# Kernel tuning notes

Hardware: AMD Instinct MI355X
Metric: run time of the kernel (lower is better)

The kernel has to match this reference:

```python
import math
import jax
import jax.numpy as jnp
import numpy as np

N_ATOMS = 5000
N_EDGES = 100000
FEAT = 128
BERN_K = 16
R_CUT = 5.0
EPS = 1e-15


def _swish(x, a, b):
    # learnable swish: alpha * x * sigmoid(beta * x)
    return a * x * jax.nn.sigmoid(b * x)


def _y_all(r_ij, r, l):
    """Real spherical harmonics of the unit vector r_ij/r, all m in [-l, l]."""
    x, y, z = r_ij[:, 0], r_ij[:, 1], r_ij[:, 2]
    if l == 0:
        return jnp.ones((r_ij.shape[0], 1), r_ij.dtype)
    if l == 1:
        return jnp.stack([y, z, x], axis=1) / r
    s3 = math.sqrt(3.0)
    r2 = (r * r)[:, 0]
    return jnp.stack(
        [s3 * x * y, s3 * y * z, 1.5 * z * z - 0.5 * r2, s3 * x * z, 0.5 * s3 * (x * x - y * y)],
        axis=1,
    ) / r2[:, None]


def _rho_k(r, gamma, K):
    """Bernstein radial basis b_{k,K-1}(exp(-gamma r)) times SpookyNet smooth cutoff."""
    rr = r[:, 0]
    g = jnp.maximum(gamma, 0.0)  # gamma.clamp(0)
    e = jnp.exp(-g * rr)[:, None]  # [E,1]
    k = jnp.arange(K)
    binom = jnp.asarray([math.comb(K - 1, i) for i in range(K)], dtype=r.dtype)
    bern = binom * e ** k * (1.0 - e) ** (K - 1 - k)  # [E,K]
    safe = jnp.where(rr < R_CUT, (R_CUT - rr) * (R_CUT + rr), 1.0)
    fcut = jnp.where(rr < R_CUT, jnp.exp(-rr * rr / safe), 0.0)
    return bern * fcut[:, None]


def _forward(xyz, x_tilde, rm_W1, rm_b1, rm_W2, rm_b2, rm_W3, rm_b3,
             rl_W1, rl_b1, rl_W2, rl_b2, rl_W3, rl_b3,
             G_s, G_p, G_d, P_1, P_2, D_1, D_2,
             gamma_s, gamma_p, gamma_d, sw_alpha, sw_beta, nbrs):
    n = xyz.shape[0]
    sw = lambda t, i: _swish(t, sw_alpha[i], sw_beta[i])
    # batched pre-activation linear over channel dim c
    bl = lambda W, b, t: jnp.einsum('cij,cnj->cni', W, t) + b[:, None, :]

    # BatchedResidualMLP on x_tilde repeated over 4 channels
    x4 = jnp.broadcast_to(x_tilde, (4,) + x_tilde.shape)  # [4,N,F]
    h = x4 + bl(rm_W2, rm_b2, sw(bl(rm_W1, rm_b1, sw(x4, 0)), 1))
    res_outs = x4 + bl(rm_W3, rm_b3, sw(h, 2))  # [4,N,F]

    i0, i1 = nbrs[:, 0], nbrs[:, 1]
    r_ij = xyz[i1] - xyz[i0]  # [E,3]
    r = jnp.sqrt((r_ij ** 2 + EPS).sum(-1, keepdims=True))  # stable norm, [E,1]
    K = G_s.shape[1]

    def quant(l, gamma, G, res_out):
        # g: [E,K,2l+1] = rho_k outer y_lm
        g = _rho_k(r, gamma, K)[:, :, None] * _y_all(r_ij, r, l)[:, None, :]
        mm = jnp.einsum('fk,ekm->efm', G, g)  # [E,F,2l+1]
        per = res_out[i1][:, :, None] * mm
        return jax.ops.segment_sum(per, i0, num_segments=n)  # scatter_add -> [N,F,2l+1]

    q_s = quant(0, gamma_s, G_s, res_outs[1])
    q_p = quant(1, gamma_p, G_p, res_outs[2])
    q_d = quant(2, gamma_d, G_d, res_outs[3])

    def inner(q, M1, M2):
        t1 = jnp.einsum('ij,njm->nim', M1, q)
        t2 = jnp.einsum('ij,njm->nim', M2, q)
        return (t1 * t2).sum(-1)

    inp = res_outs[0] + q_s[:, :, 0] + inner(q_p, P_1, P_2) + inner(q_d, D_1, D_2)

    # ResidualMLP (note: no outer skip, matching the torch code)
    lin = lambda W, b, t: t @ W.T + b
    h2 = inp + lin(rl_W2, rl_b2, sw(lin(rl_W1, rl_b1, sw(inp, 3)), 4))
    return lin(rl_W3, rl_b3, sw(h2, 5))


def setup_inputs():
    key = jax.random.key(0)
    ks = jax.random.split(key, 24)
    p = lambda k, shape: jax.random.normal(k, shape, dtype=jnp.float32) * 0.1
    F, K = FEAT, BERN_K
    return {
        'xyz': jax.random.normal(ks[0], (N_ATOMS, 3), jnp.float32) * 3.0,
        'x_tilde': jax.random.normal(ks[1], (N_ATOMS, F), jnp.float32),
        'nbrs': jax.random.randint(ks[2], (N_EDGES, 2), 0, N_ATOMS),
        'rm_W1': p(ks[3], (4, F, F)), 'rm_b1': p(ks[4], (4, F)),
        'rm_W2': p(ks[5], (4, F, F)), 'rm_b2': p(ks[6], (4, F)),
        'rm_W3': p(ks[7], (4, F, F)), 'rm_b3': p(ks[8], (4, F)),
        'rl_W1': p(ks[9], (F, F)), 'rl_b1': p(ks[10], (F,)),
        'rl_W2': p(ks[11], (F, F)), 'rl_b2': p(ks[12], (F,)),
        'rl_W3': p(ks[13], (F, F)), 'rl_b3': p(ks[14], (F,)),
        'G_s': p(ks[15], (F, K)), 'G_p': p(ks[16], (F, K)), 'G_d': p(ks[17], (F, K)),
        'P_1': p(ks[18], (F, F)), 'P_2': p(ks[19], (F, F)),
        'D_1': p(ks[20], (F, F)), 'D_2': p(ks[21], (F, F)),
        'gamma_s': jnp.asarray(0.5, jnp.float32),
        'gamma_p': jnp.asarray(0.5, jnp.float32),
        'gamma_d': jnp.asarray(0.5, jnp.float32),
        'sw_alpha': jnp.ones((6,), jnp.float32),
        'sw_beta': jnp.full((6,), 1.702, jnp.float32),
    }


def reference(xyz, x_tilde, nbrs, rm_W1, rm_b1, rm_W2, rm_b2, rm_W3, rm_b3,
              rl_W1, rl_b1, rl_W2, rl_b2, rl_W3, rl_b3,
              G_s, G_p, G_d, P_1, P_2, D_1, D_2,
              gamma_s, gamma_p, gamma_d, sw_alpha, sw_beta):
    return _forward(xyz, x_tilde, rm_W1, rm_b1, rm_W2, rm_b2, rm_W3, rm_b3,
                    rl_W1, rl_b1, rl_W2, rl_b2, rl_W3, rl_b3,
                    G_s, G_p, G_d, P_1, P_2, D_1, D_2,
                    gamma_s, gamma_p, gamma_d, sw_alpha, sw_beta, nbrs)
```

## Files before the change

### kernel.cpp

```cpp
#include <hip/hip_runtime.h>
#include <hip/hip_bf16.h>
#include <math.h>

#define NA 5000
#define NE 100000
#define F 128
#define KB 16
#define RCUT 5.0f
#define RECW 28
#define QCAP 40

typedef long long i64;
typedef __attribute__((ext_vector_type(8))) short bf16x8;
typedef __attribute__((ext_vector_type(4))) float f32x4;

__device__ __forceinline__ float swish_f(float t, float a, float b){
    return a * t / (1.0f + __expf(-b * t));
}
__device__ __forceinline__ float bf2f(unsigned short u){
    return __uint_as_float(((unsigned)u) << 16);
}
__device__ __forceinline__ unsigned short f2bf(float x){
    unsigned b = __float_as_uint(x);
    return (unsigned short)((b + 0x8000u) >> 16);
}
__device__ __forceinline__ unsigned pack2(float a, float b){
    return (unsigned)f2bf(a) | ((unsigned)f2bf(b) << 16);
}
__device__ __forceinline__ int swz(int row, int byte_in_row){
    return row * 256 + (byte_in_row ^ ((row & 7) << 4));
}

template<int MT>
__device__ __forceinline__ void gemm_stage(const unsigned short* __restrict__ Wb,
                                           const short* act_lds, f32x4 (&acc)[MT][2],
                                           int lane, int wave)
{
    bf16x8 B[2][4], A[MT][4];
    const int cl = lane & 15, kh = lane >> 4;
    #pragma unroll
    for (int ntl = 0; ntl < 2; ++ntl){
        const unsigned short* wp = Wb + (i64)(wave * 32 + ntl * 16 + cl) * F + kh * 8;
        #pragma unroll
        for (int kb = 0; kb < 4; ++kb)
            B[ntl][kb] = *(const bf16x8*)(wp + kb * 32);
    }
    #pragma unroll
    for (int mt = 0; mt < MT; ++mt){
        int row = mt * 16 + cl;
        #pragma unroll
        for (int kb = 0; kb < 4; ++kb)
            A[mt][kb] = *(const bf16x8*)((const char*)act_lds + swz(row, kb * 64 + kh * 16));
    }
    #pragma unroll
    for (int mt = 0; mt < MT; ++mt)
        #pragma unroll
        for (int ntl = 0; ntl < 2; ++ntl)
            #pragma unroll
            for (int kb = 0; kb < 4; ++kb)
                acc[mt][ntl] = __builtin_amdgcn_mfma_f32_16x16x32_bf16(
                    A[mt][kb], B[ntl][kb], acc[mt][ntl], 0, 0, 0);
}

__device__ __forceinline__ void epi_lds(f32x4 acc[2][2], const float* __restrict__ bc,
                                        const float* resid_lds, int use_resid,
                                        float aS, float bS, short* act_lds,
                                        int lane, int wave)
{
    const int cl = lane & 15, r4 = (lane >> 4) * 4;
    #pragma unroll
    for (int ntl = 0; ntl < 2; ++ntl){
        int col = wave * 32 + ntl * 16 + cl;
        float bv = bc[col];
        #pragma unroll
        for (int mt = 0; mt < 2; ++mt){
            #pragma unroll
            for (int j = 0; j < 4; ++j){
                int row = mt * 16 + r4 + j;
                float z = acc[mt][ntl][j] + bv;
                if (use_resid) z += resid_lds[row * 132 + col];
                z = swish_f(z, aS, bS);
                *(short*)((char*)act_lds + swz(row, col * 2)) = (short)f2bf(z);
            }
        }
    }
}

__device__ __forceinline__ void basis16(float r, float g, float fcut, float* b){
    const float C[KB] = {1.f,15.f,105.f,455.f,1365.f,3003.f,5005.f,6435.f,
                         6435.f,5005.f,3003.f,1365.f,455.f,105.f,15.f,1.f};
    float e = __expf(-fmaxf(g, 0.f) * r);
    float one = 1.f - e;
    float ep = 1.f;
    #pragma unroll
    for (int k = 0; k < KB; ++k){ b[k] = C[k] * ep * fcut; ep *= e; }
    float op = 1.f;
    #pragma unroll
    for (int k = KB-1; k >= 0; --k){ b[k] *= op; op *= one; }
}

__device__ __forceinline__ void prep_edge_block(
    int ebid, const float* __restrict__ xyz, const int* __restrict__ nbrs,
    int* __restrict__ fill, int* __restrict__ idx,
    const float* __restrict__ gs, const float* __restrict__ gp,
    const float* __restrict__ gd, float* __restrict__ rec)
{
    int e = ebid * 256 + threadIdx.x;
    if (e >= NE) return;
    int i0 = nbrs[2*e], i1 = nbrs[2*e+1];
    float dx = xyz[3*i1]   - xyz[3*i0];
    float dy = xyz[3*i1+1] - xyz[3*i0+1];
    float dz = xyz[3*i1+2] - xyz[3*i0+2];
    float r2 = dx*dx + dy*dy + dz*dz + 3e-15f;
    float r = sqrtf(r2);
    if (r >= RCUT) return;
    int slot = atomicAdd(&fill[i0], 1);
    if (slot < QCAP) idx[i0 * QCAP + slot] = e;
    float* R = rec + (i64)e * RECW;
    float ir = 1.f / r;
    R[0] = __int_as_float(i1);
    R[1] = dx * ir; R[2] = dy * ir; R[3] = dz * ir;
    float fcut = __expf(-r2 / ((RCUT - r) * (RCUT + r)));
    float bs[KB], bp[KB], bd[KB];
    basis16(r, gs[0], fcut, bs);
    basis16(r, gp[0], fcut, bp);
    basis16(r, gd[0], fcut, bd);
    unsigned* RW = (unsigned*)(R + 4);
    #pragma unroll
    for (int k = 0; k < 8; ++k) RW[k]      = pack2(bs[2*k], bs[2*k+1]);
    #pragma unroll
    for (int k = 0; k < 8; ++k) RW[8 + k]  = pack2(bp[2*k], bp[2*k+1]);
    #pragma unroll
    for (int k = 0; k < 8; ++k) RW[16 + k] = pack2(bd[2*k], bd[2*k+1]);
}

template<int S0, int S1, int S2, int ADD2, int ADD3, int ADDPART, int PREP, int CH, int RESB>
__global__ __launch_bounds__(256)
void mlp3_mfma(const float* __restrict__ in, const unsigned short* __restrict__ part,
               const unsigned short* __restrict__ W1b, const float* __restrict__ b1,
               const unsigned short* __restrict__ W2b, const float* __restrict__ b2,
               const unsigned short* __restrict__ W3b, const float* __restrict__ b3,
               float* __restrict__ out, unsigned short* __restrict__ resb,
               const float* __restrict__ sw_a, const float* __restrict__ sw_b, int n,
               const float* __restrict__ xyz, const int* __restrict__ nbrs,
               int* __restrict__ fill, int* __restrict__ idx,
               const float* __restrict__ gs, const float* __restrict__ gp,
               const float* __restrict__ gd, float* __restrict__ rec)
{
    if (PREP && blockIdx.y >= CH){
        int ebid = (blockIdx.y - CH) * gridDim.x + blockIdx.x;
        if (ebid < (NE + 255) / 256)
            prep_edge_block(ebid, xyz, nbrs, fill, idx, gs, gp, gd, rec);
        return;
    }

    __shared__ short act_lds[32 * 128];
    __shared__ float resid_lds[32 * 132];
    const int tid = threadIdx.x;
    const int lane = tid & 63, wave = tid >> 6;
    const int c = blockIdx.y;
    const int a0 = blockIdx.x * 32;
    const i64 S = (i64)NA * F;

    const unsigned short* Wc1 = W1b + (i64)c * F * F;
    const unsigned short* Wc2 = W2b + (i64)c * F * F;
    const unsigned short* Wc3 = W3b + (i64)c * F * F;
    const float* bc1 = b1 + c * F;
    const float* bc2 = b2 + c * F;
    const float* bc3 = b3 + c * F;

    {
        float aS = sw_a[S0], bS = sw_b[S0];
        #pragma unroll
        for (int it = 0; it < 4; ++it){
            int ch = tid + it * 256;
            int row = ch >> 5, j4 = ch & 31;
            int g = a0 + row;
            float4 v = make_float4(0.f, 0.f, 0.f, 0.f);
            if (g < n){
                v = *(const float4*)(in + (i64)g * F + j4 * 4);
                if (ADDPART){
                    #pragma unroll
                    for (int m = 0; m < 8; ++m){
                        ushort4 u = *(const ushort4*)(part + (i64)m * S + (i64)g * F + j4 * 4);
                        v.x += bf2f(u.x); v.y += bf2f(u.y);
                        v.z += bf2f(u.z); v.w += bf2f(u.w);
                    }
                }
            }
            *(float4*)&resid_lds[row * 132 + j4 * 4] = v;
            uint2 p;
            p.x = pack2(swish_f(v.x, aS, bS), swish_f(v.y, aS, bS));
            p.y = pack2(swish_f(v.z, aS, bS), swish_f(v.w, aS, bS));
            *(uint2*)((char*)act_lds + swz(row, j4 * 8)) = p;
        }
    }
    __syncthreads();

    f32x4 acc[2][2];
    #pragma unroll
    for (int a = 0; a < 2; ++a){ acc[a][0] = (f32x4){0,0,0,0}; acc[a][1] = (f32x4){0,0,0,0}; }
    gemm_stage<2>(Wc1, act_lds, acc, lane, wave);
    __syncthreads();
    epi_lds(acc, bc1, resid_lds, 0, sw_a[S1], sw_b[S1], act_lds, lane, wave);
    __syncthreads();

    #pragma unroll
    for (int a = 0; a < 2; ++a){ acc[a][0] = (f32x4){0,0,0,0}; acc[a][1] = (f32x4){0,0,0,0}; }
    gemm_stage<2>(Wc2, act_lds, acc, lane, wave);
    __syncthreads();
    epi_lds(acc, bc2, resid_lds, ADD2, sw_a[S2], sw_b[S2], act_lds, lane, wave);
    __syncthreads();

    #pragma unroll
    for (int a = 0; a < 2; ++a){ acc[a][0] = (f32x4){0,0,0,0}; acc[a][1] = (f32x4){0,0,0,0}; }
    gemm_stage<2>(Wc3, act_lds, acc, lane, wave);
    {
        const int cl = lane & 15, r4 = (lane >> 4) * 4;
        #pragma unroll
        for (int ntl = 0; ntl < 2; ++ntl){
            int col = wave * 32 + ntl * 16 + cl;
            float bv = bc3[col];
            #pragma unroll
            for (int mt = 0; mt < 2; ++mt){
                #pragma unroll
                for (int j = 0; j < 4; ++j){
                    int row = mt * 16 + r4 + j;
                    int g = a0 + row;
                    if (g >= n) continue;
                    float z = acc[mt][ntl][j] + bv;
                    if (ADD3) z += resid_lds[row * 132 + col];
                    if (RESB && c > 0)
                        resb[(i64)(c - 1) * S + (i64)g * F + col] = f2bf(z);
                    else
                        out[(i64)g * F + col] = z;
                }
            }
        }
    }
}

__global__ __launch_bounds__(256)
void bilinear_mfma(const unsigned short* __restrict__ Q,
                   const unsigned short* __restrict__ P1b, const unsigned short* __restrict__ P2b,
                   const unsigned short* __restrict__ D1b, const unsigned short* __restrict__ D2b,
                   unsigned short* __restrict__ part, int n)
{
    __shared__ short act_lds[64 * 128];
    const int tid = threadIdx.x;
    const int lane = tid & 63, wave = tid >> 6;
    const int m = blockIdx.y;
    const int a0 = blockIdx.x * 64;
    const i64 S = (i64)NA * F;
    const unsigned short* M1 = (m < 3) ? P1b : D1b;
    const unsigned short* M2 = (m < 3) ? P2b : D2b;
    const unsigned short* A = Q + (i64)m * S;

    #pragma unroll
    for (int it = 0; it < 4; ++it){
        int ch = tid + it * 256;
        int row = ch >> 4, o16 = ch & 15;
        int g = a0 + row;
        uint4 v = make_uint4(0u, 0u, 0u, 0u);
        if (g < n) v = *(const uint4*)(A + (i64)g * F + o16 * 8);
        *(uint4*)((char*)act_lds + swz(row, o16 * 16)) = v;
    }
    __syncthreads();

    f32x4 acc1[4][2], acc2[4][2];
    #pragma unroll
    for (int a = 0; a < 4; ++a){
        acc1[a][0] = (f32x4){0,0,0,0}; acc1[a][1] = (f32x4){0,0,0,0};
        acc2[a][0] = (f32x4){0,0,0,0}; acc2[a][1] = (f32x4){0,0,0,0};
    }
    gemm_stage<4>(M1, act_lds, acc1, lane, wave);
    gemm_stage<4>(M2, act_lds, acc2, lane, wave);

    const int cl = lane & 15, r4 = (lane >> 4) * 4;
    #pragma unroll
    for (int ntl = 0; ntl < 2; ++ntl){
        int col = wave * 32 + ntl * 16 + cl;
        #pragma unroll
        for (int mt = 0; mt < 4; ++mt){
            #pragma unroll
            for (int j = 0; j < 4; ++j){
                int g = a0 + mt * 16 + r4 + j;
                if (g >= n) continue;
                part[(i64)m * S + (i64)g * F + col] =
                    f2bf(acc1[mt][ntl][j] * acc2[mt][ntl][j]);
            }
        }
    }
}

__global__ __launch_bounds__(256)
void wconv(const float* s0, const float* s1, const float* s2, const float* s3,
           const float* s4, const float* s5, const float* s6, const float* s7,
           const float* s8, const float* s9, const float* g0, const float* g1,
           const float* g2, unsigned short* __restrict__ dst,
           int* __restrict__ fillz)
{
    int t = blockIdx.y;
    if (t == 0){
        for (int i = blockIdx.x * 256 + threadIdx.x; i < NA; i += 32 * 256)
            fillz[i] = 0;
    }
    const float* src; i64 off; int sz;
    if      (t == 0){ src = s0; off = 0;      sz = 65536; }
    else if (t == 1){ src = s1; off = 65536;  sz = 65536; }
    else if (t == 2){ src = s2; off = 131072; sz = 65536; }
    else if (t == 3){ src = s3; off = 196608; sz = 16384; }
    else if (t == 4){ src = s4; off = 212992; sz = 16384; }
    else if (t == 5){ src = s5; off = 229376; sz = 16384; }
    else if (t == 6){ src = s6; off = 245760; sz = 16384; }
    else if (t == 7){ src = s7; off = 262144; sz = 16384; }
    else if (t == 8){ src = s8; off = 278528; sz = 16384; }
    else if (t == 9){ src = s9; off = 294912; sz = 16384; }
    else if (t ==10){ src = g0; off = 311296; sz = 2048; }
    else if (t ==11){ src = g1; off = 313344; sz = 2048; }
    else            { src = g2; off = 315392; sz = 2048; }
    unsigned* d = (unsigned*)(dst + off);
    int pairs = sz >> 1;
    for (int p = blockIdx.x * 256 + threadIdx.x; p < pairs; p += gridDim.x * 256)
        d[p] = pack2(src[2 * p], src[2 * p + 1]);
}

__global__ __launch_bounds__(256)
void q_gather(const float* __restrict__ rec, const int* __restrict__ idx,
              const int* __restrict__ fill,
              const float* __restrict__ res0, const unsigned short* __restrict__ resb,
              const unsigned* __restrict__ Gb,
              float* __restrict__ inp, unsigned short* __restrict__ Q)
{
    const int n = blockIdx.x;
    const int tid = threadIdx.x;
    const int s = tid >> 7;
    const int f = tid & 127;
    const int lane = tid & 63, wave = tid >> 6;
    const i64 S = (i64)NA * F;

    __shared__ int   idx_s[QCAP];
    __shared__ float recs[QCAP * RECW];
    __shared__ __align__(16) char upool[12288];
    unsigned short* D = (unsigned short*)upool;
    float* red = (float*)upool;

    if (tid < QCAP) idx_s[tid] = idx[n * QCAP + tid];
    const int cnt = min(fill[n], QCAP);
    __syncthreads();
    for (int w = tid; w < cnt * RECW; w += 256){
        int j = w / RECW, o = w - j * RECW;
        recs[w] = rec[(i64)idx_s[j] * RECW + o];
    }
    __syncthreads();

    float qs = 0.f;
    float qp0=0.f, qp1=0.f, qp2=0.f;
    float qd0=0.f, qd1=0.f, qd2=0.f, qd3=0.f, qd4=0.f;
    const float s3 = 1.7320508075688772f;
    const int cl = lane & 15, kh = lane >> 4;

    for (int base = 0; base < cnt; base += 16){
        {
            int er = base + cl; if (er >= QCAP) er = 0;
            bf16x8 A[3];
            #pragma unroll
            for (int ch = 0; ch < 3; ++ch){
                if (kh < 2){
                    const unsigned* bw = (const unsigned*)&recs[er * RECW + 4];
                    union { uint4 u; bf16x8 h; } cv;
                    cv.u = *(const uint4*)(bw + ch * 8 + kh * 4);
                    A[ch] = cv.h;
                } else {
                    A[ch] = (bf16x8){0,0,0,0,0,0,0,0};
                }
            }
            #pragma unroll
            for (int ch = 0; ch < 3; ++ch){
                #pragma unroll
                for (int ct = 0; ct < 2; ++ct){
                    int fc = wave * 32 + ct * 16 + cl;
                    bf16x8 B;
                    if (kh < 2){
                        union { uint4 u; bf16x8 h; } cv;
                        cv.u = *(const uint4*)(Gb + (i64)ch * F * 8 + fc * 8 + kh * 4);
                        B = cv.h;
                    } else {
                        B = (bf16x8){0,0,0,0,0,0,0,0};
                    }
                    f32x4 z = (f32x4){0.f, 0.f, 0.f, 0.f};
                    z = __builtin_amdgcn_mfma_f32_16x16x32_bf16(A[ch], B, z, 0, 0, 0);
                    #pragma unroll
                    for (int j = 0; j < 4; ++j)
                        D[ch * 2048 + (kh * 4 + j) * 128 + fc] = f2bf(z[j]);
                }
            }
        }
        __syncthreads();

        const int mrec = min(16, cnt - base);
        int j = s;
        float a1n = 0.f, a2n = 0.f, a3n = 0.f;
        if (j < mrec){
            int i1 = __float_as_int(recs[(base + j) * RECW]);
            a1n = bf2f(resb[(i64)i1 * F + f]);
            a2n = bf2f(resb[S + (i64)i1 * F + f]);
            a3n = bf2f(resb[2 * S + (i64)i1 * F + f]);
        }
        for (; j < mrec; j += 2){
            float a1 = a1n, a2 = a2n, a3 = a3n;
            int jn = j + 2;
            if (jn < mrec){
                int i1 = __float_as_int(recs[(base + jn) * RECW]);
                a1n = bf2f(resb[(i64)i1 * F + f]);
                a2n = bf2f(resb[S + (i64)i1 * F + f]);
                a3n = bf2f(resb[2 * S + (i64)i1 * F + f]);
            }
            const float* R = &recs[(base + j) * RECW];
            float ux = R[1], uy = R[2], uz = R[3];
            float ds = bf2f(D[0 * 2048 + j * 128 + f]);
            float dp = bf2f(D[1 * 2048 + j * 128 + f]);
            float dd = bf2f(D[2 * 2048 + j * 128 + f]);
            qs += a1 * ds;
            float tp = a2 * dp;
            qp0 += tp * uy; qp1 += tp * uz; qp2 += tp * ux;
            float td = a3 * dd;
            qd0 += td * (s3 * ux * uy);
            qd1 += td * (s3 * uy * uz);
            qd2 += td * (1.5f * uz * uz - 0.5f);
            qd3 += td * (s3 * ux * uz);
            qd4 += td * (0.5f * s3 * (ux*ux - uy*uy));
        }
        __syncthreads();
    }

    red[(s * 9 + 0) * 128 + f] = qs;
    red[(s * 9 + 1) * 128 + f] = qp0; red[(s * 9 + 2) * 128 + f] = qp1;
    red[(s * 9 + 3) * 128 + f] = qp2;
    red[(s * 9 + 4) * 128 + f] = qd0; red[(s * 9 + 5) * 128 + f] = qd1;
    red[(s * 9 + 6) * 128 + f] = qd2; red[(s * 9 + 7) * 128 + f] = qd3;
    red[(s * 9 + 8) * 128 + f] = qd4;
    __syncthreads();
    if (s == 0){
        float sums[9];
        #pragma unroll
        for (int i = 0; i < 9; ++i)
            sums[i] = red[(0 * 9 + i) * 128 + f] + red[(1 * 9 + i) * 128 + f];
        inp[(i64)n*F + f] = res0[(i64)n*F + f] + sums[0];
        #pragma unroll
        for (int mm = 0; mm < 8; ++mm)
            Q[(i64)mm * S + (i64)n*F + f] = f2bf(sums[1 + mm]);
    }
}

extern "C" void kernel_launch(void* const* d_in, const int* in_sizes, int n_in,
                              void* d_out, int out_size, void* d_ws, size_t ws_size,
                              hipStream_t stream)
{
    const float* xyz     = (const float*)d_in[0];
    const float* x_tilde = (const float*)d_in[1];
    const int*   nbrs    = (const int*)d_in[2];
    const float* rm_W1 = (const float*)d_in[3],  *rm_b1 = (const float*)d_in[4];
    const float* rm_W2 = (const float*)d_in[5],  *rm_b2 = (const float*)d_in[6];
    const float* rm_W3 = (const float*)d_in[7],  *rm_b3 = (const float*)d_in[8];
    const float* rl_W1 = (const float*)d_in[9],  *rl_b1 = (const float*)d_in[10];
    const float* rl_W2 = (const float*)d_in[11], *rl_b2 = (const float*)d_in[12];
    const float* rl_W3 = (const float*)d_in[13], *rl_b3 = (const float*)d_in[14];
    const float* G_s = (const float*)d_in[15], *G_p = (const float*)d_in[16], *G_d = (const float*)d_in[17];
    const float* P_1 = (const float*)d_in[18], *P_2 = (const float*)d_in[19];
    const float* D_1 = (const float*)d_in[20], *D_2 = (const float*)d_in[21];
    const float* gamma_s = (const float*)d_in[22], *gamma_p = (const float*)d_in[23], *gamma_d = (const float*)d_in[24];
    const float* sw_a = (const float*)d_in[25], *sw_b = (const float*)d_in[26];

    const i64 S = (i64)NA * F;
    float* res0 = (float*)d_ws;
    unsigned short* resb = (unsigned short*)(res0 + S);
    float* inp  = (float*)(resb + 3 * S);
    unsigned short* Q = (unsigned short*)(inp + S);
    float* rec  = (float*)(Q + 8 * S);
    unsigned short* part = (unsigned short*)rec;
    int* fill   = (int*)(rec + (i64)NE * RECW);
    int* idx    = fill + NA + 8;
    unsigned short* Wb = (unsigned short*)(idx + NA * QCAP);

    const int NT = (NA + 31) / 32;

    wconv<<<dim3(32, 13), 256, 0, stream>>>(rm_W1, rm_W2, rm_W3, rl_W1, rl_W2, rl_W3,
                                            P_1, P_2, D_1, D_2, G_s, G_p, G_d, Wb, fill);

    mlp3_mfma<0,1,2,1,1,0,1,4,1><<<dim3(NT, 7), 256, 0, stream>>>(
        x_tilde, (const unsigned short*)nullptr,
        Wb + 0, rm_b1, Wb + 65536, rm_b2, Wb + 131072, rm_b3,
        res0, resb, sw_a, sw_b, NA,
        xyz, nbrs, fill, idx, gamma_s, gamma_p, gamma_d, rec);

    q_gather<<<NA, 256, 0, stream>>>(rec, idx, fill, res0, resb,
                                     (const unsigned*)(Wb + 311296), inp, Q);

    bilinear_mfma<<<dim3((NA + 63) / 64, 8), 256, 0, stream>>>(
        Q, Wb + 245760, Wb + 262144, Wb + 278528, Wb + 294912, part, NA);

    mlp3_mfma<3,4,5,1,0,1,0,1,0><<<dim3(NT, 1), 256, 0, stream>>>(
        inp, part,
        Wb + 196608, rl_b1, Wb + 212992, rl_b2, Wb + 229376, rl_b3,
        (float*)d_out, nullptr, sw_a, sw_b, NA,
        nullptr, nullptr, nullptr, nullptr, nullptr, nullptr, nullptr, nullptr);
}
```

Measured before the change: 74.25 us.

## Process two atoms per q_gather block and drop the cross-half reduction

q_gather now assigns two atoms per 256-thread block, one per 128-thread half, instead of splitting one atom's neighbour records across two halves. Each half walks its own atom's records in chunks of 8, so the shared-memory partial-sum reduction and its extra barrier go away, and the grid is halved. In exchange, each thread runs a serial chain of twice as many records. The two halves are also tied to the longer of the two neighbour counts, and half of each MFMA's K lanes and rows now go unused.

Measured after the change: 81.06 us. +9.2%, slower.

```diff
diff --git a/kernel.cpp b/kernel.cpp
--- a/kernel.cpp
+++ b/kernel.cpp
@@ -332,27 +332,35 @@
               const unsigned* __restrict__ Gb,
               float* __restrict__ inp, unsigned short* __restrict__ Q)
 {
-    const int n = blockIdx.x;
+    const int bx = blockIdx.x;
     const int tid = threadIdx.x;
-    const int s = tid >> 7;
-    const int f = tid & 127;
-    const int lane = tid & 63, wave = tid >> 6;
+    const int pa = tid >> 7;
+    const int f  = tid & 127;
+    const int n  = bx * 2 + pa;
+    const int lane = tid & 63;
+    const int wv = (tid >> 6) & 1;
     const i64 S = (i64)NA * F;
 
-    __shared__ int   idx_s[QCAP];
-    __shared__ float recs[QCAP * RECW];
-    __shared__ __align__(16) char upool[12288];
-    unsigned short* D = (unsigned short*)upool;
-    float* red = (float*)upool;
-
-    if (tid < QCAP) idx_s[tid] = idx[n * QCAP + tid];
-    const int cnt = min(fill[n], QCAP);
-    __syncthreads();
-    for (int w = tid; w < cnt * RECW; w += 256){
+    __shared__ int   idx_s[2][QCAP];
+    __shared__ float recs[2][QCAP * RECW];
+    __shared__ unsigned short D[2][3 * 8 * 128];
+
+    if (tid < 2 * QCAP) ((int*)idx_s)[tid] = idx[(i64)bx * 2 * QCAP + tid];
+    const int cnt0 = min(fill[bx * 2], QCAP);
+    const int cnt1 = min(fill[bx * 2 + 1], QCAP);
+    __syncthreads();
+    for (int w = tid; w < cnt0 * RECW; w += 256){
         int j = w / RECW, o = w - j * RECW;
-        recs[w] = rec[(i64)idx_s[j] * RECW + o];
-    }
-    __syncthreads();
+        recs[0][w] = rec[(i64)idx_s[0][j] * RECW + o];
+    }
+    for (int w = tid; w < cnt1 * RECW; w += 256){
+        int j = w / RECW, o = w - j * RECW;
+        recs[1][w] = rec[(i64)idx_s[1][j] * RECW + o];
+    }
+    __syncthreads();
+
+    const int cnt = pa ? cnt1 : cnt0;
+    const int nch = (max(cnt0, cnt1) + 7) >> 3;
 
     float qs = 0.f;
     float qp0=0.f, qp1=0.f, qp2=0.f;
@@ -360,14 +368,15 @@
     const float s3 = 1.7320508075688772f;
     const int cl = lane & 15, kh = lane >> 4;
 
-    for (int base = 0; base < cnt; base += 16){
+    for (int ci = 0; ci < nch; ++ci){
+        const int base = ci * 8;
         {
             int er = base + cl; if (er >= QCAP) er = 0;
             bf16x8 A[3];
             #pragma unroll
             for (int ch = 0; ch < 3; ++ch){
                 if (kh < 2){
-                    const unsigned* bw = (const unsigned*)&recs[er * RECW + 4];
+                    const unsigned* bw = (const unsigned*)&recs[pa][er * RECW + 4];
                     union { uint4 u; bf16x8 h; } cv;
                     cv.u = *(const uint4*)(bw + ch * 8 + kh * 4);
                     A[ch] = cv.h;
@@ -378,8 +387,8 @@
             #pragma unroll
             for (int ch = 0; ch < 3; ++ch){
                 #pragma unroll
-                for (int ct = 0; ct < 2; ++ct){
-                    int fc = wave * 32 + ct * 16 + cl;
+                for (int ct = 0; ct < 4; ++ct){
+                    int fc = wv * 64 + ct * 16 + cl;
                     bf16x8 B;
                     if (kh < 2){
                         union { uint4 u; bf16x8 h; } cv;
@@ -390,37 +399,39 @@
                     }
                     f32x4 z = (f32x4){0.f, 0.f, 0.f, 0.f};
                     z = __builtin_amdgcn_mfma_f32_16x16x32_bf16(A[ch], B, z, 0, 0, 0);
-                    #pragma unroll
-                    for (int j = 0; j < 4; ++j)
-                        D[ch * 2048 + (kh * 4 + j) * 128 + fc] = f2bf(z[j]);
+                    if (kh < 2){
+                        #pragma unroll
+                        for (int j = 0; j < 4; ++j)
+                            D[pa][ch * 1024 + (kh * 4 + j) * 128 + fc] = f2bf(z[j]);
+                    }
                 }
             }
         }
         __syncthreads();
 
-        const int mrec = min(16, cnt - base);
-        int j = s;
+        const int mrec = min(8, cnt - base);
+        int j = 0;
         float a1n = 0.f, a2n = 0.f, a3n = 0.f;
         if (j < mrec){
-            int i1 = __float_as_int(recs[(base + j) * RECW]);
+            int i1 = __float_as_int(recs[pa][(base + j) * RECW]);
             a1n = bf2f(resb[(i64)i1 * F + f]);
             a2n = bf2f(resb[S + (i64)i1 * F + f]);
             a3n = bf2f(resb[2 * S + (i64)i1 * F + f]);
         }
-        for (; j < mrec; j += 2){
+        for (; j < mrec; ++j){
             float a1 = a1n, a2 = a2n, a3 = a3n;
-            int jn = j + 2;
+            int jn = j + 1;
             if (jn < mrec){
-                int i1 = __float_as_int(recs[(base + jn) * RECW]);
+                int i1 = __float_as_int(recs[pa][(base + jn) * RECW]);
                 a1n = bf2f(resb[(i64)i1 * F + f]);
                 a2n = bf2f(resb[S + (i64)i1 * F + f]);
                 a3n = bf2f(resb[2 * S + (i64)i1 * F + f]);
             }
-            const float* R = &recs[(base + j) * RECW];
+            const float* R = &recs[pa][(base + j) * RECW];
             float ux = R[1], uy = R[2], uz = R[3];
-            float ds = bf2f(D[0 * 2048 + j * 128 + f]);
-            float dp = bf2f(D[1 * 2048 + j * 128 + f]);
-            float dd = bf2f(D[2 * 2048 + j * 128 + f]);
+            float ds = bf2f(D[pa][0 * 1024 + j * 128 + f]);
+            float dp = bf2f(D[pa][1 * 1024 + j * 128 + f]);
+            float dd = bf2f(D[pa][2 * 1024 + j * 128 + f]);
             qs += a1 * ds;
             float tp = a2 * dp;
             qp0 += tp * uy; qp1 += tp * uz; qp2 += tp * ux;
@@ -434,23 +445,15 @@
         __syncthreads();
     }
 
-    red[(s * 9 + 0) * 128 + f] = qs;
-    red[(s * 9 + 1) * 128 + f] = qp0; red[(s * 9 + 2) * 128 + f] = qp1;
-    red[(s * 9 + 3) * 128 + f] = qp2;
-    red[(s * 9 + 4) * 128 + f] = qd0; red[(s * 9 + 5) * 128 + f] = qd1;
-    red[(s * 9 + 6) * 128 + f] = qd2; red[(s * 9 + 7) * 128 + f] = qd3;
-    red[(s * 9 + 8) * 128 + f] = qd4;
-    __syncthreads();
-    if (s == 0){
-        float sums[9];
-        #pragma unroll
-        for (int i = 0; i < 9; ++i)
-            sums[i] = red[(0 * 9 + i) * 128 + f] + red[(1 * 9 + i) * 128 + f];
-        inp[(i64)n*F + f] = res0[(i64)n*F + f] + sums[0];
-        #pragma unroll
-        for (int mm = 0; mm < 8; ++mm)
-            Q[(i64)mm * S + (i64)n*F + f] = f2bf(sums[1 + mm]);
-    }
+    inp[(i64)n * F + f] = res0[(i64)n * F + f] + qs;
+    Q[0*S + (i64)n*F + f] = f2bf(qp0);
+    Q[1*S + (i64)n*F + f] = f2bf(qp1);
+    Q[2*S + (i64)n*F + f] = f2bf(qp2);
+    Q[3*S + (i64)n*F + f] = f2bf(qd0);
+    Q[4*S + (i64)n*F + f] = f2bf(qd1);
+    Q[5*S + (i64)n*F + f] = f2bf(qd2);
+    Q[6*S + (i64)n*F + f] = f2bf(qd3);
+    Q[7*S + (i64)n*F + f] = f2bf(qd4);
 }
 
 extern "C" void kernel_launch(void* const* d_in, const int* in_sizes, int n_in,
@@ -494,8 +497,8 @@
         res0, resb, sw_a, sw_b, NA,
         xyz, nbrs, fill, idx, gamma_s, gamma_p, gamma_d, rec);
 
-    q_gather<<<NA, 256, 0, stream>>>(rec, idx, fill, res0, resb,
-                                     (const unsigned*)(Wb + 311296), inp, Q);
+    q_gather<<<NA / 2, 256, 0, stream>>>(rec, idx, fill, res0, resb,
+                                         (const unsigned*)(Wb + 311296), inp, Q);
 
     bilinear_mfma<<<dim3((NA + 63) / 64, 8), 256, 0, stream>>>(
         Q, Wb + 245760, Wb + 262144, Wb + 278528, Wb + 294912, part, NA);
```
